# Kernel tuning notes

Hardware: AMD Instinct MI355X
Metric: run time of the kernel (lower is better)

Reference implementation:

```python
import jax, jax.numpy as jnp
import numpy as np

# SOM hyperparameters (match init_kwargs)
M, N = 64, 64
NODES = M * N
FEATS = 256
BATCH = 1024
LR = 0.5
RADIUS_FACTOR = 1.1
TOTAL_ITER = 100000
SIGMA = max(M, N) * RADIUS_FACTOR


def setup_inputs() -> dict:
    key = jax.random.key(0)
    k1, k2 = jax.random.split(key)
    x = jax.random.uniform(k1, (BATCH, FEATS), dtype=jnp.float32)
    map_w = jax.random.uniform(k2, (NODES, FEATS), dtype=jnp.float32)
    return {"x": x, "map_w": map_w, "iteration": 0}


def _grid_locs():
    ii, jj = jnp.meshgrid(jnp.arange(M), jnp.arange(N), indexing='ij')
    return jnp.stack([ii.ravel(), jj.ravel()], axis=1)  # (NODES, 2) int32


def reference(x, map_w, iteration):
    B = x.shape[0]
    # ---- feedforward: squared distances (B, NODES) via GEMM expansion,
    # avoiding the (B, NODES, FEATS) broadcast the TF code materializes.
    x2 = jnp.sum(x * x, axis=1, keepdims=True)          # (B, 1)
    w2 = jnp.sum(map_w * map_w, axis=1)                  # (NODES,)
    sqd = x2 + w2[None, :] - 2.0 * (x @ map_w.T)         # (B, NODES)
    bmu_indices = jnp.argmin(sqd, axis=1)                # (B,)

    # ---- backprop: neighborhood-weighted codebook update
    locs = _grid_locs()                                  # (NODES, 2)
    bmu_locs = locs[bmu_indices]                         # (B, 2)
    # grid distance^2 between every node and each sample's BMU: (B, NODES)
    d2 = jnp.sum((locs[None, :, :] - bmu_locs[:, None, :]) ** 2, axis=2).astype(jnp.float32)

    lambda_g = TOTAL_ITER / SIGMA
    decay = jnp.exp(jnp.float32(-float(iteration) / lambda_g))
    radius = SIGMA * decay + 1e-6
    lr = LR * decay

    impact = jnp.exp(-d2 / (2.0 * radius * radius))
    in_radius = (jnp.sqrt(d2) <= radius).astype(jnp.float32)
    lr_op = impact * in_radius * lr                      # (B, NODES)

    # weight_update[n,d] = sum_b lr_op[b,n] * (x[b,d] - map_w[n,d])
    # computed without the (B, NODES, FEATS) intermediate:
    upd = (jnp.einsum('bn,bd->nd', lr_op, x) - lr_op.sum(axis=0)[:, None] * map_w) / B
    new_map = map_w + upd
    return new_map, bmu_indices
```

## Files before the change

kernel.cpp:

```cpp
#include <hip/hip_runtime.h>
#include <math.h>

#define NODES 4096
#define FEATS 256
#define BATCH 1024
#define LR_C 0.5f
#define SIGMA_C 70.4f

typedef _Float16 f16x8 __attribute__((ext_vector_type(8)));
typedef float floatx4 __attribute__((ext_vector_type(4)));

__device__ __forceinline__ void get_params(int it, float& lr, float& r2, float& i2r2) {
    float decay = __expf(-(float)it * (SIGMA_C / 100000.0f));
    float radius = SIGMA_C * decay + 1e-6f;
    lr = LR_C * decay;
    r2 = radius * radius;
    i2r2 = 1.0f / (2.0f * r2);
}

__device__ __forceinline__ unsigned fkey(float f) {
    unsigned u = __float_as_uint(f);
    return (u & 0x80000000u) ? ~u : (u | 0x80000000u);
}
__device__ __forceinline__ float funkey(unsigned k) {
    unsigned u = (k & 0x80000000u) ? (k & 0x7fffffffu) : ~k;
    return __uint_as_float(u);
}
__device__ __forceinline__ unsigned long long shfl_xor_u64(unsigned long long v, int mask) {
    unsigned lo = (unsigned)v, hi = (unsigned)(v >> 32);
    lo = __shfl_xor(lo, mask, 64);
    hi = __shfl_xor(hi, mask, 64);
    return ((unsigned long long)hi << 32) | lo;
}

__global__ __launch_bounds__(256) void k_prep(const float* __restrict__ Wm, const float* __restrict__ X,
                                              _Float16* __restrict__ Wh, float* __restrict__ w2,
                                              _Float16* __restrict__ Xh, _Float16* __restrict__ XT,
                                              unsigned long long* __restrict__ gmin) {
    __shared__ _Float16 T[64][72];
    const int t = threadIdx.x;
    const int blk = blockIdx.x;
    const int wave = t >> 6, lane = t & 63;
#pragma unroll
    for (int rr = 0; rr < 2; ++rr) {
        int row = blk * 8 + wave * 2 + rr;
        float4 v = *(const float4*)&Wm[(size_t)row * FEATS + lane * 4];
        union { _Float16 h[4]; float2 f2; } u;
        u.h[0] = (_Float16)v.x; u.h[1] = (_Float16)v.y;
        u.h[2] = (_Float16)v.z; u.h[3] = (_Float16)v.w;
        *(float2*)&Wh[(size_t)row * FEATS + lane * 4] = u.f2;
        float s = v.x * v.x + v.y * v.y + v.z * v.z + v.w * v.w;
#pragma unroll
        for (int off = 32; off > 0; off >>= 1) s += __shfl_down(s, off, 64);
        if (lane == 0) w2[row] = s;
    }
    if (blk < 4) gmin[blk * 256 + t] = 0xFFFFFFFFFFFFFFFFULL;
    if (blk < 64) {
        const int b0 = (blk & 15) * 64, d0 = (blk >> 4) * 64;
        {
            const int bl = t >> 2, dq = (t & 3) * 16;
            union { _Float16 h[16]; float4 q[2]; } u;
#pragma unroll
            for (int c = 0; c < 4; ++c) {
                float4 v = *(const float4*)&X[(size_t)(b0 + bl) * FEATS + d0 + dq + c * 4];
                u.h[c * 4 + 0] = (_Float16)v.x; u.h[c * 4 + 1] = (_Float16)v.y;
                u.h[c * 4 + 2] = (_Float16)v.z; u.h[c * 4 + 3] = (_Float16)v.w;
            }
            *(float4*)&Xh[(size_t)(b0 + bl) * FEATS + d0 + dq] = u.q[0];
            *(float4*)&Xh[(size_t)(b0 + bl) * FEATS + d0 + dq + 8] = u.q[1];
#pragma unroll
            for (int c = 0; c < 16; ++c) T[bl][dq + c] = u.h[c];
        }
        __syncthreads();
        {
            const int dl = t >> 2, bq = (t & 3) * 16;
            union { _Float16 h[16]; float4 q[2]; } u;
#pragma unroll
            for (int c = 0; c < 16; ++c) u.h[c] = T[bq + c][dl];
            *(float4*)&XT[(size_t)(d0 + dl) * BATCH + b0 + bq] = u.q[0];
            *(float4*)&XT[(size_t)(d0 + dl) * BATCH + b0 + bq + 8] = u.q[1];
        }
    }
}

__global__ __launch_bounds__(256) void k_gemm1min(const _Float16* __restrict__ Xh, const _Float16* __restrict__ Wh,
                                                  const float* __restrict__ w2, _Float16* __restrict__ Sd,
                                                  unsigned long long* __restrict__ gmin) {
    __shared__ _Float16 As[64][40];
    __shared__ _Float16 Bs[64][40];
    __shared__ unsigned long long rowmin[64][2];
    const int n0 = blockIdx.x * 64;
    const int b0 = blockIdx.y * 64;
    const int t = threadIdx.x;
    const int wave = t >> 6, lane = t & 63;
    const int wm = wave & 1, wn = wave >> 1;
    const int lm = lane & 15, quad = lane >> 4;
    const int srow = t >> 2, skoff = (t & 3) * 8;
    floatx4 acc[2][2] = {};
    for (int k0 = 0; k0 < FEATS; k0 += 32) {
        *(float4*)&As[srow][skoff] = *(const float4*)&Xh[(size_t)(b0 + srow) * FEATS + k0 + skoff];
        *(float4*)&Bs[srow][skoff] = *(const float4*)&Wh[(size_t)(n0 + srow) * FEATS + k0 + skoff];
        __syncthreads();
        f16x8 af0 = *(f16x8*)&As[wm * 32 + lm][quad * 8];
        f16x8 af1 = *(f16x8*)&As[wm * 32 + 16 + lm][quad * 8];
        f16x8 bf0 = *(f16x8*)&Bs[wn * 32 + lm][quad * 8];
        f16x8 bf1 = *(f16x8*)&Bs[wn * 32 + 16 + lm][quad * 8];
        acc[0][0] = __builtin_amdgcn_mfma_f32_16x16x32_f16(af0, bf0, acc[0][0], 0, 0, 0);
        acc[0][1] = __builtin_amdgcn_mfma_f32_16x16x32_f16(af0, bf1, acc[0][1], 0, 0, 0);
        acc[1][0] = __builtin_amdgcn_mfma_f32_16x16x32_f16(af1, bf0, acc[1][0], 0, 0, 0);
        acc[1][1] = __builtin_amdgcn_mfma_f32_16x16x32_f16(af1, bf1, acc[1][1], 0, 0, 0);
        __syncthreads();
    }
    const int col0 = n0 + wn * 32 + lm, col1 = col0 + 16;
    const float w20 = w2[col0], w21 = w2[col1];
#pragma unroll
    for (int i = 0; i < 2; ++i) {
#pragma unroll
        for (int r = 0; r < 4; ++r) {
            int row = b0 + wm * 32 + i * 16 + quad * 4 + r;
            float va = w20 - 2.0f * acc[i][0][r];
            float vb = w21 - 2.0f * acc[i][1][r];
            Sd[(size_t)row * NODES + col0] = (_Float16)va;
            Sd[(size_t)row * NODES + col1] = (_Float16)vb;
            unsigned long long ka = ((unsigned long long)fkey(va) << 32) | (unsigned)col0;
            unsigned long long kb = ((unsigned long long)fkey(vb) << 32) | (unsigned)col1;
            unsigned long long m = ka < kb ? ka : kb;
#pragma unroll
            for (int mk = 1; mk < 16; mk <<= 1) {
                unsigned long long o = shfl_xor_u64(m, mk);
                if (o < m) m = o;
            }
            if (lm == 0) rowmin[wm * 32 + i * 16 + quad * 4 + r][wn] = m;
        }
    }
    __syncthreads();
    if (t < 64) {
        unsigned long long v = rowmin[t][0];
        if (rowmin[t][1] < v) v = rowmin[t][1];
        atomicMin(&gmin[b0 + t], v);
    }
}

__global__ __launch_bounds__(256) void k_refine(const _Float16* __restrict__ Sd, const float* __restrict__ X,
                                                const float* __restrict__ Wm, const float* __restrict__ w2,
                                                const unsigned long long* __restrict__ gmin,
                                                int* __restrict__ bmu, float* __restrict__ out1) {
    __shared__ int cand[128];
    __shared__ int cnt;
    __shared__ unsigned long long wbest[4];
    const int b = blockIdx.x;
    const int t = threadIdx.x;
    const int wave = t >> 6, lane = t & 63;
    if (t == 0) cnt = 0;
    if (t < 4) wbest[t] = 0xFFFFFFFFFFFFFFFFULL;
    __syncthreads();
    const _Float16* row = Sd + (size_t)b * NODES;
    const float thr = funkey((unsigned)(gmin[b] >> 32)) + 0.4f;
#pragma unroll
    for (int j = 0; j < 2; ++j) {
        f16x8 h = *(const f16x8*)&row[j * 2048 + t * 8];
#pragma unroll
        for (int u = 0; u < 8; ++u) {
            if ((float)h[u] <= thr) {
                int p = atomicAdd(&cnt, 1);
                if (p < 128) cand[p] = j * 2048 + t * 8 + u;
            }
        }
    }
    __syncthreads();
    const int C = cnt < 128 ? cnt : 128;
    float4 xv = *(const float4*)&X[(size_t)b * FEATS + lane * 4];
    unsigned long long best = 0xFFFFFFFFFFFFFFFFULL;
    for (int c = wave; c < C; c += 4) {
        int n = cand[c];
        float4 wv = *(const float4*)&Wm[(size_t)n * FEATS + lane * 4];
        float d = xv.x * wv.x + xv.y * wv.y + xv.z * wv.z + xv.w * wv.w;
#pragma unroll
        for (int off = 32; off > 0; off >>= 1) d += __shfl_down(d, off, 64);
        if (lane == 0) {
            float ex = w2[n] - 2.0f * d;
            unsigned long long k = ((unsigned long long)fkey(ex) << 32) | (unsigned)n;
            if (k < best) best = k;
        }
    }
    if (lane == 0) wbest[wave] = best;
    __syncthreads();
    if (t == 0) {
        unsigned long long bb = wbest[0];
#pragma unroll
        for (int w = 1; w < 4; ++w) if (wbest[w] < bb) bb = wbest[w];
        int idx = (int)(bb & 0xFFFFFFFFULL);
        bmu[b] = idx;
        out1[b] = (float)idx;
    }
}

__global__ __launch_bounds__(256) void k_lrop(const int* __restrict__ bmu, const int* __restrict__ itp,
                                              _Float16* __restrict__ lrT, float* __restrict__ Svec) {
    __shared__ int bmu_s[1024];
    __shared__ float texp[64];
    __shared__ float red4[4];
    const int t = threadIdx.x;
#pragma unroll
    for (int j = 0; j < 4; ++j) bmu_s[t + j * 256] = bmu[t + j * 256];
    float lr, r2, i2r2;
    get_params(itp[0], lr, r2, i2r2);
    if (t < 64) texp[t] = __expf(-(float)(t * t) * i2r2);
    __syncthreads();
    const int n = blockIdx.x * 2 + (t >> 7);
    const int b0 = (t & 127) * 8;
    const int ni = n >> 6, nj = n & 63;
    float s = 0.0f;
    union { _Float16 h[8]; float4 q; } u;
#pragma unroll
    for (int c = 0; c < 8; ++c) {
        int m = bmu_s[b0 + c];
        int di = ni - (m >> 6); di = di < 0 ? -di : di;
        int dj = nj - (m & 63); dj = dj < 0 ? -dj : dj;
        int d2 = di * di + dj * dj;
        float val = ((float)d2 <= r2) ? lr * texp[di] * texp[dj] : 0.0f;
        u.h[c] = (_Float16)val;
        s += val;
    }
    *(float4*)&lrT[(size_t)n * BATCH + b0] = u.q;
    const int lane = t & 63, wave = t >> 6;
#pragma unroll
    for (int off = 32; off > 0; off >>= 1) s += __shfl_down(s, off, 64);
    if (lane == 0) red4[wave] = s;
    __syncthreads();
    if (t < 2) Svec[blockIdx.x * 2 + t] = red4[2 * t] + red4[2 * t + 1];
}

__global__ __launch_bounds__(256) void k_gemm2c(const _Float16* __restrict__ lrT, const _Float16* __restrict__ XT,
                                                const float* __restrict__ Svec, const float* __restrict__ Wm,
                                                float* __restrict__ out0) {
    __shared__ _Float16 As[32][40];
    __shared__ _Float16 Bs[64][40];
    __shared__ float Svl[32];
    const int d0 = blockIdx.x * 64;
    const int n0 = blockIdx.y * 32;
    const int t = threadIdx.x;
    const int wave = t >> 6, lane = t & 63;
    const int wm = wave & 1, wn = wave >> 1;
    const int lm = lane & 15, quad = lane >> 4;
    const int srow = t >> 2, skoff = (t & 3) * 8;
    if (t < 32) Svl[t] = Svec[n0 + t];
    floatx4 acc0 = {}, acc1 = {};
    for (int k0 = 0; k0 < BATCH; k0 += 32) {
        if (t < 128)
            *(float4*)&As[srow][skoff] = *(const float4*)&lrT[(size_t)(n0 + srow) * BATCH + k0 + skoff];
        *(float4*)&Bs[srow][skoff] = *(const float4*)&XT[(size_t)(d0 + srow) * BATCH + k0 + skoff];
        __syncthreads();
        f16x8 af = *(f16x8*)&As[wm * 16 + lm][quad * 8];
        f16x8 bf0 = *(f16x8*)&Bs[wn * 32 + lm][quad * 8];
        f16x8 bf1 = *(f16x8*)&Bs[wn * 32 + 16 + lm][quad * 8];
        acc0 = __builtin_amdgcn_mfma_f32_16x16x32_f16(af, bf0, acc0, 0, 0, 0);
        acc1 = __builtin_amdgcn_mfma_f32_16x16x32_f16(af, bf1, acc1, 0, 0, 0);
        __syncthreads();
    }
    const float invB = 1.0f / (float)BATCH;
#pragma unroll
    for (int r = 0; r < 4; ++r) {
        int rowN = n0 + wm * 16 + quad * 4 + r;
        float cc = 1.0f - Svl[rowN - n0] * invB;
        int col0 = d0 + wn * 32 + lm;
        int col1 = col0 + 16;
        out0[(size_t)rowN * FEATS + col0] = Wm[(size_t)rowN * FEATS + col0] * cc + acc0[r] * invB;
        out0[(size_t)rowN * FEATS + col1] = Wm[(size_t)rowN * FEATS + col1] * cc + acc1[r] * invB;
    }
}

extern "C" void kernel_launch(void* const* d_in, const int* in_sizes, int n_in,
                              void* d_out, int out_size, void* d_ws, size_t ws_size,
                              hipStream_t stream) {
    const float* X = (const float*)d_in[0];
    const float* Wm = (const float*)d_in[1];
    const int* itp = (const int*)d_in[2];
    float* out0 = (float*)d_out;
    float* out1 = out0 + (size_t)NODES * FEATS;

    char* ws = (char*)d_ws;
    float* w2       = (float*)(ws + 0);
    _Float16* Xh    = (_Float16*)(ws + 16384);
    _Float16* XT    = (_Float16*)(ws + 540672);
    _Float16* Wh    = (_Float16*)(ws + 1064960);
    int* bmu        = (int*)(ws + 3162112);
    unsigned long long* gmin = (unsigned long long*)(ws + 3166208);
    float* Svec     = (float*)(ws + 3174400);
    _Float16* Sd    = (_Float16*)(ws + 3190784);
    _Float16* lrT   = (_Float16*)(ws + 3190784);

    k_prep<<<512, 256, 0, stream>>>(Wm, X, Wh, w2, Xh, XT, gmin);
    k_gemm1min<<<dim3(64, 16), 256, 0, stream>>>(Xh, Wh, w2, Sd, gmin);
    k_refine<<<1024, 256, 0, stream>>>(Sd, X, Wm, w2, gmin, bmu, out1);
    k_lrop<<<2048, 256, 0, stream>>>(bmu, itp, lrT, Svec);
    k_gemm2c<<<dim3(4, 128), 256, 0, stream>>>(lrT, XT, Svec, Wm, out0);
}
```

Baseline: 108.3 us.

## Replace fp16 distance matrix and refine pass with split-fp16 GEMM argmin

Splits X and W into fp16 hi and lo parts and computes the distance GEMM with three MFMAs per tile (hi*hi, hi*lo, lo*hi), giving near-fp32 accuracy. The argmin can then be taken straight from the GEMM, so the fp16 distance matrix write and the candidate-refine kernel are dropped, and BMU indices are read directly from gmin in the lr-op kernel. The second GEMM now stages K=128 per shared-memory load instead of 32, which cuts barriers. In exchange, GEMM1 does three times the MFMA work and loads twice the operand bytes, and ties or near-ties may resolve differently than an exact fp32 comparison.

```diff
diff --git a/kernel.cpp b/kernel.cpp
--- a/kernel.cpp
+++ b/kernel.cpp
@@ -22,10 +22,6 @@
     unsigned u = __float_as_uint(f);
     return (u & 0x80000000u) ? ~u : (u | 0x80000000u);
 }
-__device__ __forceinline__ float funkey(unsigned k) {
-    unsigned u = (k & 0x80000000u) ? (k & 0x7fffffffu) : ~k;
-    return __uint_as_float(u);
-}
 __device__ __forceinline__ unsigned long long shfl_xor_u64(unsigned long long v, int mask) {
     unsigned lo = (unsigned)v, hi = (unsigned)(v >> 32);
     lo = __shfl_xor(lo, mask, 64);
@@ -34,8 +30,10 @@
 }
 
 __global__ __launch_bounds__(256) void k_prep(const float* __restrict__ Wm, const float* __restrict__ X,
-                                              _Float16* __restrict__ Wh, float* __restrict__ w2,
-                                              _Float16* __restrict__ Xh, _Float16* __restrict__ XT,
+                                              _Float16* __restrict__ Whi, _Float16* __restrict__ Wlo,
+                                              float* __restrict__ w2,
+                                              _Float16* __restrict__ Xhi, _Float16* __restrict__ Xlo,
+                                              _Float16* __restrict__ XT,
                                               unsigned long long* __restrict__ gmin) {
     __shared__ _Float16 T[64][72];
     const int t = threadIdx.x;
@@ -45,10 +43,15 @@
     for (int rr = 0; rr < 2; ++rr) {
         int row = blk * 8 + wave * 2 + rr;
         float4 v = *(const float4*)&Wm[(size_t)row * FEATS + lane * 4];
-        union { _Float16 h[4]; float2 f2; } u;
-        u.h[0] = (_Float16)v.x; u.h[1] = (_Float16)v.y;
-        u.h[2] = (_Float16)v.z; u.h[3] = (_Float16)v.w;
-        *(float2*)&Wh[(size_t)row * FEATS + lane * 4] = u.f2;
+        union { _Float16 h[4]; float2 f2; } uh, ul;
+        uh.h[0] = (_Float16)v.x; uh.h[1] = (_Float16)v.y;
+        uh.h[2] = (_Float16)v.z; uh.h[3] = (_Float16)v.w;
+        ul.h[0] = (_Float16)(v.x - (float)uh.h[0]);
+        ul.h[1] = (_Float16)(v.y - (float)uh.h[1]);
+        ul.h[2] = (_Float16)(v.z - (float)uh.h[2]);
+        ul.h[3] = (_Float16)(v.w - (float)uh.h[3]);
+        *(float2*)&Whi[(size_t)row * FEATS + lane * 4] = uh.f2;
+        *(float2*)&Wlo[(size_t)row * FEATS + lane * 4] = ul.f2;
         float s = v.x * v.x + v.y * v.y + v.z * v.z + v.w * v.w;
 #pragma unroll
         for (int off = 32; off > 0; off >>= 1) s += __shfl_down(s, off, 64);
@@ -59,17 +62,23 @@
         const int b0 = (blk & 15) * 64, d0 = (blk >> 4) * 64;
         {
             const int bl = t >> 2, dq = (t & 3) * 16;
-            union { _Float16 h[16]; float4 q[2]; } u;
+            union { _Float16 h[16]; float4 q[2]; } uh, ul;
 #pragma unroll
             for (int c = 0; c < 4; ++c) {
                 float4 v = *(const float4*)&X[(size_t)(b0 + bl) * FEATS + d0 + dq + c * 4];
-                u.h[c * 4 + 0] = (_Float16)v.x; u.h[c * 4 + 1] = (_Float16)v.y;
-                u.h[c * 4 + 2] = (_Float16)v.z; u.h[c * 4 + 3] = (_Float16)v.w;
+                uh.h[c * 4 + 0] = (_Float16)v.x; uh.h[c * 4 + 1] = (_Float16)v.y;
+                uh.h[c * 4 + 2] = (_Float16)v.z; uh.h[c * 4 + 3] = (_Float16)v.w;
+                ul.h[c * 4 + 0] = (_Float16)(v.x - (float)uh.h[c * 4 + 0]);
+                ul.h[c * 4 + 1] = (_Float16)(v.y - (float)uh.h[c * 4 + 1]);
+                ul.h[c * 4 + 2] = (_Float16)(v.z - (float)uh.h[c * 4 + 2]);
+                ul.h[c * 4 + 3] = (_Float16)(v.w - (float)uh.h[c * 4 + 3]);
             }
-            *(float4*)&Xh[(size_t)(b0 + bl) * FEATS + d0 + dq] = u.q[0];
-            *(float4*)&Xh[(size_t)(b0 + bl) * FEATS + d0 + dq + 8] = u.q[1];
-#pragma unroll
-            for (int c = 0; c < 16; ++c) T[bl][dq + c] = u.h[c];
+            *(float4*)&Xhi[(size_t)(b0 + bl) * FEATS + d0 + dq] = uh.q[0];
+            *(float4*)&Xhi[(size_t)(b0 + bl) * FEATS + d0 + dq + 8] = uh.q[1];
+            *(float4*)&Xlo[(size_t)(b0 + bl) * FEATS + d0 + dq] = ul.q[0];
+            *(float4*)&Xlo[(size_t)(b0 + bl) * FEATS + d0 + dq + 8] = ul.q[1];
+#pragma unroll
+            for (int c = 0; c < 16; ++c) T[bl][dq + c] = uh.h[c];
         }
         __syncthreads();
         {
@@ -83,11 +92,14 @@
     }
 }
 
-__global__ __launch_bounds__(256) void k_gemm1min(const _Float16* __restrict__ Xh, const _Float16* __restrict__ Wh,
-                                                  const float* __restrict__ w2, _Float16* __restrict__ Sd,
+__global__ __launch_bounds__(256) void k_gemm1min(const _Float16* __restrict__ Xhi, const _Float16* __restrict__ Xlo,
+                                                  const _Float16* __restrict__ Whi, const _Float16* __restrict__ Wlo,
+                                                  const float* __restrict__ w2,
                                                   unsigned long long* __restrict__ gmin) {
-    __shared__ _Float16 As[64][40];
-    __shared__ _Float16 Bs[64][40];
+    __shared__ _Float16 Ah[64][40];
+    __shared__ _Float16 Al[64][40];
+    __shared__ _Float16 Bh[64][40];
+    __shared__ _Float16 Bl[64][40];
     __shared__ unsigned long long rowmin[64][2];
     const int n0 = blockIdx.x * 64;
     const int b0 = blockIdx.y * 64;
@@ -98,17 +110,28 @@
     const int srow = t >> 2, skoff = (t & 3) * 8;
     floatx4 acc[2][2] = {};
     for (int k0 = 0; k0 < FEATS; k0 += 32) {
-        *(float4*)&As[srow][skoff] = *(const float4*)&Xh[(size_t)(b0 + srow) * FEATS + k0 + skoff];
-        *(float4*)&Bs[srow][skoff] = *(const float4*)&Wh[(size_t)(n0 + srow) * FEATS + k0 + skoff];
-        __syncthreads();
-        f16x8 af0 = *(f16x8*)&As[wm * 32 + lm][quad * 8];
-        f16x8 af1 = *(f16x8*)&As[wm * 32 + 16 + lm][quad * 8];
-        f16x8 bf0 = *(f16x8*)&Bs[wn * 32 + lm][quad * 8];
-        f16x8 bf1 = *(f16x8*)&Bs[wn * 32 + 16 + lm][quad * 8];
-        acc[0][0] = __builtin_amdgcn_mfma_f32_16x16x32_f16(af0, bf0, acc[0][0], 0, 0, 0);
-        acc[0][1] = __builtin_amdgcn_mfma_f32_16x16x32_f16(af0, bf1, acc[0][1], 0, 0, 0);
-        acc[1][0] = __builtin_amdgcn_mfma_f32_16x16x32_f16(af1, bf0, acc[1][0], 0, 0, 0);
-        acc[1][1] = __builtin_amdgcn_mfma_f32_16x16x32_f16(af1, bf1, acc[1][1], 0, 0, 0);
+        *(float4*)&Ah[srow][skoff] = *(const float4*)&Xhi[(size_t)(b0 + srow) * FEATS + k0 + skoff];
+        *(float4*)&Al[srow][skoff] = *(const float4*)&Xlo[(size_t)(b0 + srow) * FEATS + k0 + skoff];
+        *(float4*)&Bh[srow][skoff] = *(const float4*)&Whi[(size_t)(n0 + srow) * FEATS + k0 + skoff];
+        *(float4*)&Bl[srow][skoff] = *(const float4*)&Wlo[(size_t)(n0 + srow) * FEATS + k0 + skoff];
+        __syncthreads();
+        f16x8 ah[2], al[2], bh[2], bl[2];
+        ah[0] = *(f16x8*)&Ah[wm * 32 + lm][quad * 8];
+        ah[1] = *(f16x8*)&Ah[wm * 32 + 16 + lm][quad * 8];
+        al[0] = *(f16x8*)&Al[wm * 32 + lm][quad * 8];
+        al[1] = *(f16x8*)&Al[wm * 32 + 16 + lm][quad * 8];
+        bh[0] = *(f16x8*)&Bh[wn * 32 + lm][quad * 8];
+        bh[1] = *(f16x8*)&Bh[wn * 32 + 16 + lm][quad * 8];
+        bl[0] = *(f16x8*)&Bl[wn * 32 + lm][quad * 8];
+        bl[1] = *(f16x8*)&Bl[wn * 32 + 16 + lm][quad * 8];
+#pragma unroll
+        for (int i = 0; i < 2; ++i)
+#pragma unroll
+            for (int j = 0; j < 2; ++j) {
+                acc[i][j] = __builtin_amdgcn_mfma_f32_16x16x32_f16(ah[i], bh[j], acc[i][j], 0, 0, 0);
+                acc[i][j] = __builtin_amdgcn_mfma_f32_16x16x32_f16(ah[i], bl[j], acc[i][j], 0, 0, 0);
+                acc[i][j] = __builtin_amdgcn_mfma_f32_16x16x32_f16(al[i], bh[j], acc[i][j], 0, 0, 0);
+            }
         __syncthreads();
     }
     const int col0 = n0 + wn * 32 + lm, col1 = col0 + 16;
@@ -117,11 +140,8 @@
     for (int i = 0; i < 2; ++i) {
 #pragma unroll
         for (int r = 0; r < 4; ++r) {
-            int row = b0 + wm * 32 + i * 16 + quad * 4 + r;
             float va = w20 - 2.0f * acc[i][0][r];
             float vb = w21 - 2.0f * acc[i][1][r];
-            Sd[(size_t)row * NODES + col0] = (_Float16)va;
-            Sd[(size_t)row * NODES + col1] = (_Float16)vb;
             unsigned long long ka = ((unsigned long long)fkey(va) << 32) | (unsigned)col0;
             unsigned long long kb = ((unsigned long long)fkey(vb) << 32) | (unsigned)col1;
             unsigned long long m = ka < kb ? ka : kb;
@@ -141,73 +161,24 @@
     }
 }
 
-__global__ __launch_bounds__(256) void k_refine(const _Float16* __restrict__ Sd, const float* __restrict__ X,
-                                                const float* __restrict__ Wm, const float* __restrict__ w2,
-                                                const unsigned long long* __restrict__ gmin,
-                                                int* __restrict__ bmu, float* __restrict__ out1) {
-    __shared__ int cand[128];
-    __shared__ int cnt;
-    __shared__ unsigned long long wbest[4];
-    const int b = blockIdx.x;
-    const int t = threadIdx.x;
-    const int wave = t >> 6, lane = t & 63;
-    if (t == 0) cnt = 0;
-    if (t < 4) wbest[t] = 0xFFFFFFFFFFFFFFFFULL;
-    __syncthreads();
-    const _Float16* row = Sd + (size_t)b * NODES;
-    const float thr = funkey((unsigned)(gmin[b] >> 32)) + 0.4f;
-#pragma unroll
-    for (int j = 0; j < 2; ++j) {
-        f16x8 h = *(const f16x8*)&row[j * 2048 + t * 8];
-#pragma unroll
-        for (int u = 0; u < 8; ++u) {
-            if ((float)h[u] <= thr) {
-                int p = atomicAdd(&cnt, 1);
-                if (p < 128) cand[p] = j * 2048 + t * 8 + u;
-            }
-        }
-    }
-    __syncthreads();
-    const int C = cnt < 128 ? cnt : 128;
-    float4 xv = *(const float4*)&X[(size_t)b * FEATS + lane * 4];
-    unsigned long long best = 0xFFFFFFFFFFFFFFFFULL;
-    for (int c = wave; c < C; c += 4) {
-        int n = cand[c];
-        float4 wv = *(const float4*)&Wm[(size_t)n * FEATS + lane * 4];
-        float d = xv.x * wv.x + xv.y * wv.y + xv.z * wv.z + xv.w * wv.w;
-#pragma unroll
-        for (int off = 32; off > 0; off >>= 1) d += __shfl_down(d, off, 64);
-        if (lane == 0) {
-            float ex = w2[n] - 2.0f * d;
-            unsigned long long k = ((unsigned long long)fkey(ex) << 32) | (unsigned)n;
-            if (k < best) best = k;
-        }
-    }
-    if (lane == 0) wbest[wave] = best;
-    __syncthreads();
-    if (t == 0) {
-        unsigned long long bb = wbest[0];
-#pragma unroll
-        for (int w = 1; w < 4; ++w) if (wbest[w] < bb) bb = wbest[w];
-        int idx = (int)(bb & 0xFFFFFFFFULL);
-        bmu[b] = idx;
-        out1[b] = (float)idx;
-    }
-}
-
-__global__ __launch_bounds__(256) void k_lrop(const int* __restrict__ bmu, const int* __restrict__ itp,
-                                              _Float16* __restrict__ lrT, float* __restrict__ Svec) {
+__global__ __launch_bounds__(256) void k_lropB(const unsigned long long* __restrict__ gmin,
+                                               const int* __restrict__ itp,
+                                               _Float16* __restrict__ lrT, float* __restrict__ Svec,
+                                               float* __restrict__ out1) {
     __shared__ int bmu_s[1024];
     __shared__ float texp[64];
     __shared__ float red4[4];
     const int t = threadIdx.x;
-#pragma unroll
-    for (int j = 0; j < 4; ++j) bmu_s[t + j * 256] = bmu[t + j * 256];
+    const int blk = blockIdx.x;
+#pragma unroll
+    for (int j = 0; j < 4; ++j)
+        bmu_s[t + j * 256] = (int)(gmin[t + j * 256] & 0xFFFFFFFFULL);
     float lr, r2, i2r2;
     get_params(itp[0], lr, r2, i2r2);
     if (t < 64) texp[t] = __expf(-(float)(t * t) * i2r2);
     __syncthreads();
-    const int n = blockIdx.x * 2 + (t >> 7);
+    if (blk < 4) out1[blk * 256 + t] = (float)bmu_s[blk * 256 + t];
+    const int n = blk * 2 + (t >> 7);
     const int b0 = (t & 127) * 8;
     const int ni = n >> 6, nj = n & 63;
     float s = 0.0f;
@@ -228,14 +199,14 @@
     for (int off = 32; off > 0; off >>= 1) s += __shfl_down(s, off, 64);
     if (lane == 0) red4[wave] = s;
     __syncthreads();
-    if (t < 2) Svec[blockIdx.x * 2 + t] = red4[2 * t] + red4[2 * t + 1];
+    if (t < 2) Svec[blk * 2 + t] = red4[2 * t] + red4[2 * t + 1];
 }
 
 __global__ __launch_bounds__(256) void k_gemm2c(const _Float16* __restrict__ lrT, const _Float16* __restrict__ XT,
                                                 const float* __restrict__ Svec, const float* __restrict__ Wm,
                                                 float* __restrict__ out0) {
-    __shared__ _Float16 As[32][40];
-    __shared__ _Float16 Bs[64][40];
+    __shared__ _Float16 As[32][136];
+    __shared__ _Float16 Bs[64][136];
     __shared__ float Svl[32];
     const int d0 = blockIdx.x * 64;
     const int n0 = blockIdx.y * 32;
@@ -243,19 +214,26 @@
     const int wave = t >> 6, lane = t & 63;
     const int wm = wave & 1, wn = wave >> 1;
     const int lm = lane & 15, quad = lane >> 4;
-    const int srow = t >> 2, skoff = (t & 3) * 8;
     if (t < 32) Svl[t] = Svec[n0 + t];
+    const int arow = t >> 3, acoff = (t & 7) * 16;
+    const int brow = t >> 2, bcoff = (t & 3) * 32;
     floatx4 acc0 = {}, acc1 = {};
-    for (int k0 = 0; k0 < BATCH; k0 += 32) {
-        if (t < 128)
-            *(float4*)&As[srow][skoff] = *(const float4*)&lrT[(size_t)(n0 + srow) * BATCH + k0 + skoff];
-        *(float4*)&Bs[srow][skoff] = *(const float4*)&XT[(size_t)(d0 + srow) * BATCH + k0 + skoff];
-        __syncthreads();
-        f16x8 af = *(f16x8*)&As[wm * 16 + lm][quad * 8];
-        f16x8 bf0 = *(f16x8*)&Bs[wn * 32 + lm][quad * 8];
-        f16x8 bf1 = *(f16x8*)&Bs[wn * 32 + 16 + lm][quad * 8];
-        acc0 = __builtin_amdgcn_mfma_f32_16x16x32_f16(af, bf0, acc0, 0, 0, 0);
-        acc1 = __builtin_amdgcn_mfma_f32_16x16x32_f16(af, bf1, acc1, 0, 0, 0);
+    for (int k0 = 0; k0 < BATCH; k0 += 128) {
+        *(float4*)&As[arow][acoff] = *(const float4*)&lrT[(size_t)(n0 + arow) * BATCH + k0 + acoff];
+        *(float4*)&As[arow][acoff + 8] = *(const float4*)&lrT[(size_t)(n0 + arow) * BATCH + k0 + acoff + 8];
+#pragma unroll
+        for (int c = 0; c < 4; ++c)
+            *(float4*)&Bs[brow][bcoff + c * 8] =
+                *(const float4*)&XT[(size_t)(d0 + brow) * BATCH + k0 + bcoff + c * 8];
+        __syncthreads();
+#pragma unroll
+        for (int ks = 0; ks < 128; ks += 32) {
+            f16x8 a = *(f16x8*)&As[wm * 16 + lm][ks + quad * 8];
+            f16x8 b0 = *(f16x8*)&Bs[wn * 32 + lm][ks + quad * 8];
+            f16x8 b1 = *(f16x8*)&Bs[wn * 32 + 16 + lm][ks + quad * 8];
+            acc0 = __builtin_amdgcn_mfma_f32_16x16x32_f16(a, b0, acc0, 0, 0, 0);
+            acc1 = __builtin_amdgcn_mfma_f32_16x16x32_f16(a, b1, acc1, 0, 0, 0);
+        }
         __syncthreads();
     }
     const float invB = 1.0f / (float)BATCH;
@@ -281,18 +259,17 @@
 
     char* ws = (char*)d_ws;
     float* w2       = (float*)(ws + 0);
-    _Float16* Xh    = (_Float16*)(ws + 16384);
-    _Float16* XT    = (_Float16*)(ws + 540672);
-    _Float16* Wh    = (_Float16*)(ws + 1064960);
-    int* bmu        = (int*)(ws + 3162112);
-    unsigned long long* gmin = (unsigned long long*)(ws + 3166208);
-    float* Svec     = (float*)(ws + 3174400);
-    _Float16* Sd    = (_Float16*)(ws + 3190784);
-    _Float16* lrT   = (_Float16*)(ws + 3190784);
-
-    k_prep<<<512, 256, 0, stream>>>(Wm, X, Wh, w2, Xh, XT, gmin);
-    k_gemm1min<<<dim3(64, 16), 256, 0, stream>>>(Xh, Wh, w2, Sd, gmin);
-    k_refine<<<1024, 256, 0, stream>>>(Sd, X, Wm, w2, gmin, bmu, out1);
-    k_lrop<<<2048, 256, 0, stream>>>(bmu, itp, lrT, Svec);
+    _Float16* Xhi   = (_Float16*)(ws + 16384);
+    _Float16* Xlo   = (_Float16*)(ws + 540672);
+    _Float16* XT    = (_Float16*)(ws + 1064960);
+    _Float16* Whi   = (_Float16*)(ws + 1589248);
+    _Float16* Wlo   = (_Float16*)(ws + 3686400);
+    unsigned long long* gmin = (unsigned long long*)(ws + 5783552);
+    float* Svec     = (float*)(ws + 5791744);
+    _Float16* lrT   = (_Float16*)(ws + 5808128);
+
+    k_prep<<<512, 256, 0, stream>>>(Wm, X, Whi, Wlo, w2, Xhi, Xlo, XT, gmin);
+    k_gemm1min<<<dim3(64, 16), 256, 0, stream>>>(Xhi, Xlo, Whi, Wlo, w2, gmin);
+    k_lropB<<<2048, 256, 0, stream>>>(gmin, itp, lrT, Svec, out1);
     k_gemm2c<<<dim3(4, 128), 256, 0, stream>>>(lrT, XT, Svec, Wm, out0);
 }
```

Result: faster. 95.84 us, median of 2 (-11.5%).
